# Kernel tuning notes

Hardware: AMD Instinct MI355X
Metric: run time of the kernel (lower is better)

Reference implementation:

```python
import jax, jax.numpy as jnp
import numpy as np

LATENT = 128
K = 1024          # num_embeddings
LENGTH = 128
HID = 200         # LSTM hidden
IN = 768
COND = 1536


def setup_inputs() -> dict:
    key = jax.random.key(0)
    ks = jax.random.split(key, 16)
    B = 256
    x = jax.random.normal(ks[0], (B, 1, LENGTH, IN), dtype=jnp.float32)
    condition = jax.random.normal(ks[1], (B, 1, LENGTH, COND), dtype=jnp.float32)
    noise = jax.random.normal(ks[2], (B, IN), dtype=jnp.float32)
    s = 0.05
    # LSTM params (PyTorch gate order: i, f, g, o)
    W_ih = jax.random.normal(ks[3], (4 * HID, IN), dtype=jnp.float32) * s
    W_hh = jax.random.normal(ks[4], (4 * HID, HID), dtype=jnp.float32) * s
    b_ih = jax.random.normal(ks[5], (4 * HID,), dtype=jnp.float32) * s
    b_hh = jax.random.normal(ks[6], (4 * HID,), dtype=jnp.float32) * s
    # encoder fc: HID -> LATENT
    W_enc = jax.random.normal(ks[7], (LATENT, HID), dtype=jnp.float32) * s
    b_enc = jnp.zeros((LATENT,), dtype=jnp.float32)
    # codebook, uniform(-1/K, 1/K) as in the module
    emb = jax.random.uniform(ks[8], (K, LATENT), minval=-1.0 / K, maxval=1.0 / K, dtype=jnp.float32)
    # decoder MLP
    D1_IN = LATENT + COND + IN  # 2432
    W1 = jax.random.normal(ks[9], (200, D1_IN), dtype=jnp.float32) * s
    b1 = jnp.zeros((200,), dtype=jnp.float32)
    W2 = jax.random.normal(ks[10], (400, 200), dtype=jnp.float32) * s
    b2 = jnp.zeros((400,), dtype=jnp.float32)
    W3 = jax.random.normal(ks[11], (IN, 400), dtype=jnp.float32) * s
    b3 = jnp.zeros((IN,), dtype=jnp.float32)
    return {"x": x, "condition": condition, "noise": noise,
            "W_ih": W_ih, "W_hh": W_hh, "b_ih": b_ih, "b_hh": b_hh,
            "W_enc": W_enc, "b_enc": b_enc, "emb": emb,
            "W1": W1, "b1": b1, "W2": W2, "b2": b2, "W3": W3, "b3": b3}


def _lstm_last_h(xs, W_ih, W_hh, b_ih, b_hh):
    # xs: [B, T, IN] -> final hidden state [B, HID]
    B = xs.shape[0]
    h0 = jnp.zeros((B, HID), dtype=xs.dtype)
    c0 = jnp.zeros((B, HID), dtype=xs.dtype)
    # precompute input projections for all timesteps: [T, B, 4H]
    gates_x = jnp.einsum('bti,gi->tbg', xs, W_ih) + b_ih + b_hh

    def step(carry, gx):
        h, c = carry
        g = gx + h @ W_hh.T  # [B, 4H]
        i, f, gg, o = jnp.split(g, 4, axis=-1)
        c = jax.nn.sigmoid(f) * c + jax.nn.sigmoid(i) * jnp.tanh(gg)
        h = jax.nn.sigmoid(o) * jnp.tanh(c)
        return (h, c), None

    (h, _), _ = jax.lax.scan(step, (h0, c0), gates_x)
    return h


def reference(x, condition, noise, W_ih, W_hh, b_ih, b_hh, W_enc, b_enc, emb,
              W1, b1, W2, b2, W3, b3):
    B = x.shape[0]
    # Encoder
    xs = x.reshape(B, -1, IN)                      # [B, T, 768]
    h = _lstm_last_h(xs, W_ih, W_hh, b_ih, b_hh)   # [B, 200]
    z_e = h @ W_enc.T + b_enc                      # [B, latent]
    # VectorQuantizer: squared-distance argmin + gather
    d = (jnp.sum(z_e * z_e, axis=-1, keepdims=True)
         + jnp.sum(emb * emb, axis=1)
         - 2.0 * z_e @ emb.T)                      # [B, K]
    indices = jnp.argmin(d, axis=-1)               # [B]
    z_q = emb[indices]                             # [B, latent]
    # Decoder (forward uses z_q directly)
    L = LENGTH
    z = jnp.broadcast_to(z_q[:, None, None, :], (B, 1, L, LATENT))
    n = jnp.broadcast_to(noise[:, None, None, :], (B, 1, L, IN))
    zc = jnp.concatenate([z, condition, n], axis=-1)  # [B,1,L,2432]
    h1 = jax.nn.relu(zc @ W1.T + b1)
    h2 = jax.nn.relu(h1 @ W2.T + b2)
    out = jax.nn.sigmoid(h2 @ W3.T + b3)
    return out.reshape(-1, 1, L, IN)
```

## Files before the change

### kernel.cpp

```cpp
#include <hip/hip_runtime.h>
#include <hip/hip_fp16.h>
#include <math.h>

typedef unsigned short u16;
typedef u16 u16x8 __attribute__((ext_vector_type(8)));
typedef __bf16 bf16x8 __attribute__((ext_vector_type(8)));
typedef float f32x4 __attribute__((ext_vector_type(4)));

#define HID 200
#define G4H 800
#define TLEN 128
#define LATENT 128
#define NCODES 1024
#define DIN 768
#define DCOND 1536
#define NB 256
#define MROWS (NB * TLEN)
#define LDG 896
#define LDH1 256
#define LDH2 512
#define NOUT 768

__device__ __forceinline__ u16 f2b(float f) {
  union { float f; unsigned u; } v; v.f = f;
  unsigned r = v.u + 0x7fffu + ((v.u >> 16) & 1u);
  return (u16)(r >> 16);
}
__device__ __forceinline__ float b2f(u16 h) {
  union { unsigned u; float f; } v; v.u = ((unsigned)h) << 16;
  return v.f;
}
__device__ __forceinline__ float sigf(float x) { return 1.f / (1.f + __expf(-x)); }
__device__ __forceinline__ float tanh_fast(float x) {
  return 1.f - 2.f / (__expf(2.f * x) + 1.f);
}

__device__ __forceinline__ void gl16(const void* g, void* l) {
  __builtin_amdgcn_global_load_lds(
      (const __attribute__((address_space(1))) void*)g,
      (__attribute__((address_space(3))) void*)l, 16, 0, 0);
}

__device__ __forceinline__ unsigned cvtpk(float a, float b) {
  unsigned r;
  asm("v_cvt_pk_bf16_f32 %0, %1, %2" : "=v"(r) : "v"(a), "v"(b));
  return r;
}

__global__ void cvt_pad(const float* __restrict__ src, u16* __restrict__ dst,
                        int nr, int nc, int lds, int col0, int NRp, int KP) {
  int i = blockIdx.x * blockDim.x + threadIdx.x;
  if (i >= NRp * KP) return;
  int r = i / KP, c = i - r * KP;
  float v = (r < nr && c < nc) ? src[(size_t)r * lds + col0 + c] : 0.f;
  dst[i] = f2b(v);
}

__global__ void pad_f32(const float* __restrict__ src, float* __restrict__ dst,
                        int n, int npad) {
  int i = blockIdx.x * blockDim.x + threadIdx.x;
  if (i < npad) dst[i] = (i < n) ? src[i] : 0.f;
}

__global__ void pack_whh(const float* __restrict__ Whh, __half2* __restrict__ Wt2,
                         const float* __restrict__ b_ih, const float* __restrict__ b_hh,
                         float* __restrict__ biasc) {
  int i = blockIdx.x * blockDim.x + threadIdx.x;
  if (i < 200 * 400) {
    int k = i / 400, r = i - k * 400;
    Wt2[i] = __floats2half2_rn(Whh[(size_t)r * HID + k], Whh[(size_t)(r + 400) * HID + k]);
  }
  if (i < G4H) biasc[i] = b_ih[i] + b_hh[i];
}

enum { EPI_GATES = 0, EPI_H1 = 1, EPI_H2 = 2, EPI_OUT = 3 };

__device__ __forceinline__ f32x4 mfma16(bf16x8 a, bf16x8 b, f32x4 c) {
  return __builtin_amdgcn_mfma_f32_16x16x32_bf16(a, b, c, 0, 0, 0);
}

template<bool AF32, int EPI>
__global__ __launch_bounds__(256) void gemm_bf16(
    const void* __restrict__ Ap, const u16* __restrict__ Bp,
    void* __restrict__ Cp, int K, int ldc, const float* __restrict__ bias) {
  __shared__ __attribute__((aligned(16))) char AsRaw[AF32 ? 128 * 32 * 4 : 128 * 32 * 2];
  __shared__ __attribute__((aligned(16))) u16 Bs[128 * 32];
  float* Asf = (float*)AsRaw;
  u16* As16 = (u16*)AsRaw;

  const int t = threadIdx.x;
  const int tileN = blockIdx.x * 128;
  const int tileM = blockIdx.y * 128;
  const int l = t & 63;
  const int w = t >> 6;
  const int wr = (w >> 1) * 64;
  const int wc = (w & 1) * 64;
  const int fr = l & 15;
  const int fg = l >> 4;

  const u16* bsrc[2];
  u16* bdst[2];
#pragma unroll
  for (int j = 0; j < 2; ++j) {
    int tb = w * 1024 + j * 4096 + (t & 63) * 16;
    int row = tb >> 6, gd = (tb >> 4) & 3;
    bsrc[j] = Bp + (size_t)(tileN + row) * K + ((gd ^ ((row >> 1) & 3)) << 3);
    bdst[j] = Bs + w * 512 + j * 2048;
  }
  const float* asrcF[4];
  float* adstF[4];
  const u16* asrcH[2];
  u16* adstH[2];
  if constexpr (AF32) {
#pragma unroll
    for (int j = 0; j < 4; ++j) {
      int tb = w * 1024 + j * 4096 + (t & 63) * 16;
      int row = tb >> 7, gd = (tb >> 4) & 7;
      asrcF[j] = (const float*)Ap + (size_t)(tileM + row) * K + ((gd ^ (row & 7)) << 2);
      adstF[j] = Asf + w * 256 + j * 1024;
    }
  } else {
#pragma unroll
    for (int j = 0; j < 2; ++j) {
      int tb = w * 1024 + j * 4096 + (t & 63) * 16;
      int row = tb >> 6, gd = (tb >> 4) & 3;
      asrcH[j] = (const u16*)Ap + (size_t)(tileM + row) * K + ((gd ^ ((row >> 1) & 3)) << 3);
      adstH[j] = As16 + w * 512 + j * 2048;
    }
  }

  f32x4 acc[4][4];
#pragma unroll
  for (int m = 0; m < 4; ++m)
#pragma unroll
    for (int n = 0; n < 4; ++n) {
      f32x4 z = {0.f, 0.f, 0.f, 0.f};
      acc[m][n] = z;
    }

  for (int k0 = 0; k0 < K; k0 += 32) {
#pragma unroll
    for (int j = 0; j < 2; ++j) { gl16(bsrc[j], bdst[j]); bsrc[j] += 32; }
    if constexpr (AF32) {
#pragma unroll
      for (int j = 0; j < 4; ++j) { gl16(asrcF[j], adstF[j]); asrcF[j] += 32; }
    } else {
#pragma unroll
      for (int j = 0; j < 2; ++j) { gl16(asrcH[j], adstH[j]); asrcH[j] += 32; }
    }
    __syncthreads();

    bf16x8 av[4], bv[4];
#pragma unroll
    for (int m = 0; m < 4; ++m) {
      const int row = wr + m * 16 + fr;
      if constexpr (AF32) {
        const int g0 = (2 * fg) ^ (row & 7);
        const int g1 = (2 * fg + 1) ^ (row & 7);
        float4 p0 = *(const float4*)(Asf + row * 32 + g0 * 4);
        float4 p1 = *(const float4*)(Asf + row * 32 + g1 * 4);
        uint4 u;
        u.x = cvtpk(p0.x, p0.y); u.y = cvtpk(p0.z, p0.w);
        u.z = cvtpk(p1.x, p1.y); u.w = cvtpk(p1.z, p1.w);
        av[m] = __builtin_bit_cast(bf16x8, u);
      } else {
        const int g = fg ^ ((row >> 1) & 3);
        av[m] = __builtin_bit_cast(bf16x8, *(const u16x8*)(As16 + row * 32 + g * 8));
      }
    }
#pragma unroll
    for (int n = 0; n < 4; ++n) {
      const int row = wc + n * 16 + fr;
      const int g = fg ^ ((row >> 1) & 3);
      bv[n] = __builtin_bit_cast(bf16x8, *(const u16x8*)(Bs + row * 32 + g * 8));
    }
#pragma unroll
    for (int m = 0; m < 4; ++m)
#pragma unroll
      for (int n = 0; n < 4; ++n)
        acc[m][n] = mfma16(av[m], bv[n], acc[m][n]);
    __syncthreads();
  }

#pragma unroll
  for (int m = 0; m < 4; ++m) {
#pragma unroll
    for (int n = 0; n < 4; ++n) {
      const int gcol = tileN + wc + n * 16 + fr;
      const int growb = tileM + wr + m * 16 + fg * 4;
#pragma unroll
      for (int r = 0; r < 4; ++r) {
        const int grow = growb + r;
        float v = acc[m][n][r];
        if constexpr (EPI == EPI_GATES) {
          ((u16*)Cp)[(size_t)grow * ldc + gcol] = f2b(v);
        } else if constexpr (EPI == EPI_H1) {
          v += bias[(grow >> 7) * 256 + gcol];
          v = fmaxf(v, 0.f);
          ((u16*)Cp)[(size_t)grow * ldc + gcol] = f2b(v);
        } else if constexpr (EPI == EPI_H2) {
          v += bias[gcol];
          v = fmaxf(v, 0.f);
          ((u16*)Cp)[(size_t)grow * ldc + gcol] = f2b(v);
        } else {
          v += bias[gcol];
          ((float*)Cp)[(size_t)grow * ldc + gcol] = sigf(v);
        }
      }
    }
  }
}

__global__ __attribute__((amdgpu_flat_work_group_size(448, 448), amdgpu_waves_per_eu(2, 2)))
void lstm_enc(
    const u16* __restrict__ gates, const unsigned* __restrict__ Wt2,
    const float* __restrict__ biasc,
    const float* __restrict__ Wenc, const float* __restrict__ b_enc,
    const float* __restrict__ emb, const float* __restrict__ W1,
    const float* __restrict__ b1, const float* __restrict__ noise,
    float* __restrict__ p1) {
  __shared__ __attribute__((aligned(16))) __half sh_h[208];
  __shared__ __attribute__((aligned(16))) float sh_hf[HID];
  __shared__ float sh_g[G4H];
  __shared__ __attribute__((aligned(16))) float sh_ze[LATENT];
  __shared__ float sh_zq[LATENT];
  __shared__ float sh_rd[448];
  __shared__ int sh_ri[448];
  const int r = threadIdx.x;
  const int b = blockIdx.x;
  const bool active = (r < 400);

  unsigned wv[200];
  float biasA = 0.f, biasB = 0.f;
  if (active) {
#pragma unroll
    for (int k = 0; k < 200; ++k) wv[k] = Wt2[(size_t)k * 400 + r];
    biasA = biasc[r];
    biasB = biasc[r + 400];
  }
  if (r < HID) sh_h[r] = __float2half(0.f);
  float c = 0.f;
  float gvA = 0.f, gvB = 0.f;
  if (active) {
    gvA = b2f(gates[(size_t)(b * TLEN) * LDG + r]);
    gvB = b2f(gates[(size_t)(b * TLEN) * LDG + r + 400]);
  }
  __syncthreads();

  for (int t = 0; t < TLEN; ++t) {
    float gvA_n = 0.f, gvB_n = 0.f;
    if (active && t + 1 < TLEN) {
      gvA_n = b2f(gates[(size_t)(b * TLEN + t + 1) * LDG + r]);
      gvB_n = b2f(gates[(size_t)(b * TLEN + t + 1) * LDG + r + 400]);
    }

    if (active) {
      unsigned a0 = 0, a1 = 0, a2 = 0, a3 = 0;
      const uint4* H = (const uint4*)sh_h;
#pragma unroll
      for (int q4 = 0; q4 < 25; ++q4) {
        uint4 hv = H[q4];
        asm("v_pk_fma_f16 %0, %1, %2, %0 op_sel:[0,0,0] op_sel_hi:[1,0,1]"
            : "+v"(a0) : "v"(wv[8 * q4 + 0]), "v"(hv.x));
        asm("v_pk_fma_f16 %0, %1, %2, %0 op_sel:[0,1,0] op_sel_hi:[1,1,1]"
            : "+v"(a1) : "v"(wv[8 * q4 + 1]), "v"(hv.x));
        asm("v_pk_fma_f16 %0, %1, %2, %0 op_sel:[0,0,0] op_sel_hi:[1,0,1]"
            : "+v"(a2) : "v"(wv[8 * q4 + 2]), "v"(hv.y));
        asm("v_pk_fma_f16 %0, %1, %2, %0 op_sel:[0,1,0] op_sel_hi:[1,1,1]"
            : "+v"(a3) : "v"(wv[8 * q4 + 3]), "v"(hv.y));
        asm("v_pk_fma_f16 %0, %1, %2, %0 op_sel:[0,0,0] op_sel_hi:[1,0,1]"
            : "+v"(a0) : "v"(wv[8 * q4 + 4]), "v"(hv.z));
        asm("v_pk_fma_f16 %0, %1, %2, %0 op_sel:[0,1,0] op_sel_hi:[1,1,1]"
            : "+v"(a1) : "v"(wv[8 * q4 + 5]), "v"(hv.z));
        asm("v_pk_fma_f16 %0, %1, %2, %0 op_sel:[0,0,0] op_sel_hi:[1,0,1]"
            : "+v"(a2) : "v"(wv[8 * q4 + 6]), "v"(hv.w));
        asm("v_pk_fma_f16 %0, %1, %2, %0 op_sel:[0,1,0] op_sel_hi:[1,1,1]"
            : "+v"(a3) : "v"(wv[8 * q4 + 7]), "v"(hv.w));
      }
      __half2 s = __hadd2(__hadd2(__builtin_bit_cast(__half2, a0), __builtin_bit_cast(__half2, a1)),
                          __hadd2(__builtin_bit_cast(__half2, a2), __builtin_bit_cast(__half2, a3)));
      sh_g[r] = biasA + gvA + __low2float(s);
      sh_g[r + 400] = biasB + gvB + __high2float(s);
    }
    __syncthreads();
    if (r < HID) {
      float gi = sh_g[r], gf = sh_g[HID + r], gg = sh_g[2 * HID + r], go = sh_g[3 * HID + r];
      c = sigf(gf) * c + sigf(gi) * tanh_fast(gg);
      float h = sigf(go) * tanh_fast(c);
      sh_h[r] = __float2half(h);
      sh_hf[r] = h;
    }
    __syncthreads();
    gvA = gvA_n; gvB = gvB_n;
  }

  if (r < LATENT) {
    float z = b_enc[r];
#pragma unroll 4
    for (int k = 0; k < HID; ++k) z = fmaf(Wenc[(size_t)r * HID + k], sh_hf[k], z);
    sh_ze[r] = z;
  }
  __syncthreads();

  float best = INFINITY; int bi = 0;
  for (int k = r; k < NCODES; k += 448) {
    float d = 0.f;
#pragma unroll
    for (int q = 0; q < LATENT / 4; ++q) {
      float4 e = *(const float4*)&emb[(size_t)k * LATENT + q * 4];
      float4 z = *(const float4*)&sh_ze[q * 4];
      d += e.x * (e.x - 2.f * z.x) + e.y * (e.y - 2.f * z.y)
         + e.z * (e.z - 2.f * z.z) + e.w * (e.w - 2.f * z.w);
    }
    if (d < best) { best = d; bi = k; }
  }
  sh_rd[r] = best; sh_ri[r] = bi;
  __syncthreads();
  for (int s = 256; s > 0; s >>= 1) {
    if (r < s && r + s < 448) {
      float od = sh_rd[r + s]; int oi = sh_ri[r + s];
      if (od < sh_rd[r] || (od == sh_rd[r] && oi < sh_ri[r])) { sh_rd[r] = od; sh_ri[r] = oi; }
    }
    __syncthreads();
  }
  const int kmin = sh_ri[0];
  if (r < LATENT) sh_zq[r] = emb[(size_t)kmin * LATENT + r];
  __syncthreads();

  if (r < 256) {
    float v = 0.f;
    if (r < HID) {
      v = b1[r];
      const float* wrow = W1 + (size_t)r * 2432;
#pragma unroll 4
      for (int d = 0; d < LATENT; ++d) v = fmaf(wrow[d], sh_zq[d], v);
      const float* nz = noise + (size_t)b * DIN;
#pragma unroll 4
      for (int d = 0; d < DIN; ++d) v = fmaf(wrow[1664 + d], nz[d], v);
    }
    p1[b * 256 + r] = v;
  }
}

extern "C" void kernel_launch(void* const* d_in, const int* in_sizes, int n_in,
                              void* d_out, int out_size, void* d_ws, size_t ws_size,
                              hipStream_t stream) {
  const float* x     = (const float*)d_in[0];
  const float* cond  = (const float*)d_in[1];
  const float* noise = (const float*)d_in[2];
  const float* W_ih  = (const float*)d_in[3];
  const float* W_hh  = (const float*)d_in[4];
  const float* b_ih  = (const float*)d_in[5];
  const float* b_hh  = (const float*)d_in[6];
  const float* W_enc = (const float*)d_in[7];
  const float* b_enc = (const float*)d_in[8];
  const float* emb   = (const float*)d_in[9];
  const float* W1    = (const float*)d_in[10];
  const float* b1    = (const float*)d_in[11];
  const float* W2    = (const float*)d_in[12];
  const float* b2    = (const float*)d_in[13];
  const float* W3    = (const float*)d_in[14];
  const float* b3    = (const float*)d_in[15];

  char* ws = (char*)d_ws;
  size_t off = 0;
  auto alloc = [&](size_t bytes) -> void* {
    void* p = ws + off; off += (bytes + 255) & ~(size_t)255; return p;
  };
  u16*      W_ihb = (u16*)alloc((size_t)896 * 768 * 2);
  u16*      W1cb  = (u16*)alloc((size_t)256 * 1536 * 2);
  u16*      W2b   = (u16*)alloc((size_t)512 * 256 * 2);
  u16*      W3b   = (u16*)alloc((size_t)768 * 512 * 2);
  float*    b2p   = (float*)alloc(512 * 4);
  unsigned* Wt2   = (unsigned*)alloc((size_t)200 * 400 * 4);
  float*    biasc = (float*)alloc(G4H * 4);
  u16*      gates = (u16*)alloc((size_t)MROWS * LDG * 2);
  float*    p1    = (float*)alloc(256 * 256 * 4);
  u16*      h1    = (u16*)alloc((size_t)MROWS * LDH1 * 2);
  u16*      h2    = (u16*)alloc((size_t)MROWS * LDH2 * 2);

  cvt_pad<<<dim3((896 * 768 + 255) / 256), 256, 0, stream>>>(W_ih, W_ihb, 800, 768, 768, 0, 896, 768);
  cvt_pad<<<dim3((256 * 1536 + 255) / 256), 256, 0, stream>>>(W1, W1cb, 200, 1536, 2432, 128, 256, 1536);
  cvt_pad<<<dim3((512 * 256 + 255) / 256), 256, 0, stream>>>(W2, W2b, 400, 200, 200, 0, 512, 256);
  cvt_pad<<<dim3((768 * 512 + 255) / 256), 256, 0, stream>>>(W3, W3b, 768, 400, 400, 0, 768, 512);
  pad_f32<<<dim3(2), 256, 0, stream>>>(b2, b2p, 400, 512);
  pack_whh<<<dim3((200 * 400 + 255) / 256), 256, 0, stream>>>(W_hh, (__half2*)Wt2, b_ih, b_hh, biasc);

  gemm_bf16<true, EPI_GATES><<<dim3(LDG / 128, MROWS / 128), 256, 0, stream>>>(
      x, W_ihb, gates, 768, LDG, nullptr);

  lstm_enc<<<dim3(NB), 448, 0, stream>>>(gates, Wt2, biasc, W_enc, b_enc,
                                         emb, W1, b1, noise, p1);

  gemm_bf16<true, EPI_H1><<<dim3(LDH1 / 128, MROWS / 128), 256, 0, stream>>>(
      cond, W1cb, h1, DCOND, LDH1, p1);
  gemm_bf16<false, EPI_H2><<<dim3(LDH2 / 128, MROWS / 128), 256, 0, stream>>>(
      h1, W2b, h2, LDH1, LDH2, b2p);
  gemm_bf16<false, EPI_OUT><<<dim3(NOUT / 128, MROWS / 128), 256, 0, stream>>>(
      h2, W3b, (float*)d_out, LDH2, NOUT, b3);
}
```

Before: 576.4 us.

## Store LSTM recurrent weights as scaled FP8 in registers, accumulate in fp32

The recurrent weight matrix W_hh is quantized to FP8 E4M3 with a power-of-two scale of 16 instead of fp16, which halves the per-thread register footprint (100 instead of 200 VGPRs of weights). The occupancy hint is raised from 2 to 4 waves per EU, and the dot product now unpacks FP8 to fp32 and uses scalar fp32 FMAs against an fp32 hidden state. Fewer weight registers are meant to allow more concurrent waves and avoid the fp16 shared-memory copy of h. In exchange the weights lose precision, and each step runs twice as many FMA instructions plus conversion ops compared with packed fp16 math.

```diff
diff --git a/kernel.cpp b/kernel.cpp
--- a/kernel.cpp
+++ b/kernel.cpp
@@ -1,11 +1,11 @@
 #include <hip/hip_runtime.h>
-#include <hip/hip_fp16.h>
 #include <math.h>
 
 typedef unsigned short u16;
 typedef u16 u16x8 __attribute__((ext_vector_type(8)));
 typedef __bf16 bf16x8 __attribute__((ext_vector_type(8)));
 typedef float f32x4 __attribute__((ext_vector_type(4)));
+typedef float f32x2 __attribute__((ext_vector_type(2)));
 
 #define HID 200
 #define G4H 800
@@ -35,6 +35,27 @@
   return 1.f - 2.f / (__expf(2.f * x) + 1.f);
 }
 
+__device__ __forceinline__ unsigned enc_e4m3(float v) {
+  union { float f; unsigned u; } x; x.f = v;
+  unsigned s = (x.u >> 31) << 7;
+  float a = fabsf(v);
+  if (a == 0.f) return s;
+  if (a >= 448.f) return s | 0x7E;
+  int exp = (int)((x.u >> 23) & 0xFF) - 127;
+  unsigned man = (x.u >> 20) & 0x7;
+  unsigned rnd = (x.u >> 19) & 1;
+  man += rnd;
+  if (man > 7) { man = 0; exp += 1; }
+  int be = exp + 7;
+  if (be >= 16) return s | 0x7E;
+  if (be <= 0) {
+    int q = (int)(a * 512.f + 0.5f);
+    if (q > 7) q = 7;
+    return s | (unsigned)q;
+  }
+  return s | ((unsigned)be << 4) | man;
+}
+
 __device__ __forceinline__ void gl16(const void* g, void* l) {
   __builtin_amdgcn_global_load_lds(
       (const __attribute__((address_space(1))) void*)g,
@@ -62,13 +83,18 @@
   if (i < npad) dst[i] = (i < n) ? src[i] : 0.f;
 }
 
-__global__ void pack_whh(const float* __restrict__ Whh, __half2* __restrict__ Wt2,
-                         const float* __restrict__ b_ih, const float* __restrict__ b_hh,
-                         float* __restrict__ biasc) {
+__global__ void pack_whh_fp8(const float* __restrict__ Whh, unsigned* __restrict__ Wq,
+                             const float* __restrict__ b_ih, const float* __restrict__ b_hh,
+                             float* __restrict__ biasc) {
   int i = blockIdx.x * blockDim.x + threadIdx.x;
-  if (i < 200 * 400) {
-    int k = i / 400, r = i - k * 400;
-    Wt2[i] = __floats2half2_rn(Whh[(size_t)r * HID + k], Whh[(size_t)(r + 400) * HID + k]);
+  if (i < 100 * 400) {
+    int j = i / 400, r = i - j * 400;
+    int k = 2 * j;
+    unsigned b0 = enc_e4m3(16.f * Whh[(size_t)r * HID + k]);
+    unsigned b1 = enc_e4m3(16.f * Whh[(size_t)(r + 400) * HID + k]);
+    unsigned b2 = enc_e4m3(16.f * Whh[(size_t)r * HID + k + 1]);
+    unsigned b3 = enc_e4m3(16.f * Whh[(size_t)(r + 400) * HID + k + 1]);
+    Wq[i] = b0 | (b1 << 8) | (b2 << 16) | (b3 << 24);
   }
   if (i < G4H) biasc[i] = b_ih[i] + b_hh[i];
 }
@@ -211,15 +237,14 @@
   }
 }
 
-__global__ __attribute__((amdgpu_flat_work_group_size(448, 448), amdgpu_waves_per_eu(2, 2)))
+__global__ __attribute__((amdgpu_flat_work_group_size(448, 448), amdgpu_waves_per_eu(4, 4)))
 void lstm_enc(
-    const u16* __restrict__ gates, const unsigned* __restrict__ Wt2,
+    const u16* __restrict__ gates, const unsigned* __restrict__ Wq,
     const float* __restrict__ biasc,
     const float* __restrict__ Wenc, const float* __restrict__ b_enc,
     const float* __restrict__ emb, const float* __restrict__ W1,
     const float* __restrict__ b1, const float* __restrict__ noise,
     float* __restrict__ p1) {
-  __shared__ __attribute__((aligned(16))) __half sh_h[208];
   __shared__ __attribute__((aligned(16))) float sh_hf[HID];
   __shared__ float sh_g[G4H];
   __shared__ __attribute__((aligned(16))) float sh_ze[LATENT];
@@ -230,15 +255,15 @@
   const int b = blockIdx.x;
   const bool active = (r < 400);
 
-  unsigned wv[200];
+  unsigned wv[100];
   float biasA = 0.f, biasB = 0.f;
   if (active) {
 #pragma unroll
-    for (int k = 0; k < 200; ++k) wv[k] = Wt2[(size_t)k * 400 + r];
+    for (int j = 0; j < 100; ++j) wv[j] = Wq[(size_t)j * 400 + r];
     biasA = biasc[r];
     biasB = biasc[r + 400];
   }
-  if (r < HID) sh_h[r] = __float2half(0.f);
+  if (r < HID) sh_hf[r] = 0.f;
   float c = 0.f;
   float gvA = 0.f, gvB = 0.f;
   if (active) {
@@ -255,40 +280,29 @@
     }
 
     if (active) {
-      unsigned a0 = 0, a1 = 0, a2 = 0, a3 = 0;
-      const uint4* H = (const uint4*)sh_h;
-#pragma unroll
-      for (int q4 = 0; q4 < 25; ++q4) {
-        uint4 hv = H[q4];
-        asm("v_pk_fma_f16 %0, %1, %2, %0 op_sel:[0,0,0] op_sel_hi:[1,0,1]"
-            : "+v"(a0) : "v"(wv[8 * q4 + 0]), "v"(hv.x));
-        asm("v_pk_fma_f16 %0, %1, %2, %0 op_sel:[0,1,0] op_sel_hi:[1,1,1]"
-            : "+v"(a1) : "v"(wv[8 * q4 + 1]), "v"(hv.x));
-        asm("v_pk_fma_f16 %0, %1, %2, %0 op_sel:[0,0,0] op_sel_hi:[1,0,1]"
-            : "+v"(a2) : "v"(wv[8 * q4 + 2]), "v"(hv.y));
-        asm("v_pk_fma_f16 %0, %1, %2, %0 op_sel:[0,1,0] op_sel_hi:[1,1,1]"
-            : "+v"(a3) : "v"(wv[8 * q4 + 3]), "v"(hv.y));
-        asm("v_pk_fma_f16 %0, %1, %2, %0 op_sel:[0,0,0] op_sel_hi:[1,0,1]"
-            : "+v"(a0) : "v"(wv[8 * q4 + 4]), "v"(hv.z));
-        asm("v_pk_fma_f16 %0, %1, %2, %0 op_sel:[0,1,0] op_sel_hi:[1,1,1]"
-            : "+v"(a1) : "v"(wv[8 * q4 + 5]), "v"(hv.z));
-        asm("v_pk_fma_f16 %0, %1, %2, %0 op_sel:[0,0,0] op_sel_hi:[1,0,1]"
-            : "+v"(a2) : "v"(wv[8 * q4 + 6]), "v"(hv.w));
-        asm("v_pk_fma_f16 %0, %1, %2, %0 op_sel:[0,1,0] op_sel_hi:[1,1,1]"
-            : "+v"(a3) : "v"(wv[8 * q4 + 7]), "v"(hv.w));
+      float sA = 0.f, sB = 0.f;
+      const float4* H = (const float4*)sh_hf;
+#pragma unroll
+      for (int q = 0; q < 50; ++q) {
+        float4 h4 = H[q];
+        unsigned w0 = wv[2 * q], w1 = wv[2 * q + 1];
+        f32x2 lo0 = __builtin_amdgcn_cvt_pk_f32_fp8(w0, 0);
+        f32x2 hi0 = __builtin_amdgcn_cvt_pk_f32_fp8(w0, 1);
+        sA = fmaf(lo0.x, h4.x, sA); sB = fmaf(lo0.y, h4.x, sB);
+        sA = fmaf(hi0.x, h4.y, sA); sB = fmaf(hi0.y, h4.y, sB);
+        f32x2 lo1 = __builtin_amdgcn_cvt_pk_f32_fp8(w1, 0);
+        f32x2 hi1 = __builtin_amdgcn_cvt_pk_f32_fp8(w1, 1);
+        sA = fmaf(lo1.x, h4.z, sA); sB = fmaf(lo1.y, h4.z, sB);
+        sA = fmaf(hi1.x, h4.w, sA); sB = fmaf(hi1.y, h4.w, sB);
       }
-      __half2 s = __hadd2(__hadd2(__builtin_bit_cast(__half2, a0), __builtin_bit_cast(__half2, a1)),
-                          __hadd2(__builtin_bit_cast(__half2, a2), __builtin_bit_cast(__half2, a3)));
-      sh_g[r] = biasA + gvA + __low2float(s);
-      sh_g[r + 400] = biasB + gvB + __high2float(s);
+      sh_g[r] = biasA + gvA + sA * 0.0625f;
+      sh_g[r + 400] = biasB + gvB + sB * 0.0625f;
     }
     __syncthreads();
     if (r < HID) {
       float gi = sh_g[r], gf = sh_g[HID + r], gg = sh_g[2 * HID + r], go = sh_g[3 * HID + r];
       c = sigf(gf) * c + sigf(gi) * tanh_fast(gg);
-      float h = sigf(go) * tanh_fast(c);
-      sh_h[r] = __float2half(h);
-      sh_hf[r] = h;
+      sh_hf[r] = sigf(go) * tanh_fast(c);
     }
     __syncthreads();
     gvA = gvA_n; gvB = gvB_n;
@@ -372,7 +386,7 @@
   u16*      W2b   = (u16*)alloc((size_t)512 * 256 * 2);
   u16*      W3b   = (u16*)alloc((size_t)768 * 512 * 2);
   float*    b2p   = (float*)alloc(512 * 4);
-  unsigned* Wt2   = (unsigned*)alloc((size_t)200 * 400 * 4);
+  unsigned* Wq    = (unsigned*)alloc((size_t)100 * 400 * 4);
   float*    biasc = (float*)alloc(G4H * 4);
   u16*      gates = (u16*)alloc((size_t)MROWS * LDG * 2);
   float*    p1    = (float*)alloc(256 * 256 * 4);
@@ -384,12 +398,12 @@
   cvt_pad<<<dim3((512 * 256 + 255) / 256), 256, 0, stream>>>(W2, W2b, 400, 200, 200, 0, 512, 256);
   cvt_pad<<<dim3((768 * 512 + 255) / 256), 256, 0, stream>>>(W3, W3b, 768, 400, 400, 0, 768, 512);
   pad_f32<<<dim3(2), 256, 0, stream>>>(b2, b2p, 400, 512);
-  pack_whh<<<dim3((200 * 400 + 255) / 256), 256, 0, stream>>>(W_hh, (__half2*)Wt2, b_ih, b_hh, biasc);
+  pack_whh_fp8<<<dim3((100 * 400 + 255) / 256), 256, 0, stream>>>(W_hh, Wq, b_ih, b_hh, biasc);
 
   gemm_bf16<true, EPI_GATES><<<dim3(LDG / 128, MROWS / 128), 256, 0, stream>>>(
       x, W_ihb, gates, 768, LDG, nullptr);
 
-  lstm_enc<<<dim3(NB), 448, 0, stream>>>(gates, Wt2, biasc, W_enc, b_enc,
+  lstm_enc<<<dim3(NB), 448, 0, stream>>>(gates, Wq, biasc, W_enc, b_enc,
                                          emb, W1, b1, noise, p1);
 
   gemm_bf16<true, EPI_H1><<<dim3(LDH1 / 128, MROWS / 128), 256, 0, stream>>>(
```

Result: slower. 1.025 ms (+77.9%).
